# Optimization experiments

Hardware: AMD Instinct MI355X
Metric: run time of the kernel (lower is better)

## Reference

```python
import jax, jax.numpy as jnp
import numpy as np

B, V, S, H = 16384, 16, 64, 512


def setup_inputs() -> dict:
    key = jax.random.key(0)
    kx, kw, kb, kws, kbs = jax.random.split(key, 5)
    x = jax.random.normal(kx, (B, V, S), dtype=jnp.float32)
    # per-variable linear layers: weight [V, S, H], bias [V, H]
    W = jax.random.normal(kw, (V, S, H), dtype=jnp.float32) * (1.0 / np.sqrt(S))
    b = jax.random.normal(kb, (V, H), dtype=jnp.float32) * 0.01
    # variable selection linear: hidden -> V
    W_sel = jax.random.normal(kws, (H, V), dtype=jnp.float32) * (1.0 / np.sqrt(H))
    b_sel = jax.random.normal(kbs, (V,), dtype=jnp.float32) * 0.01
    return {"x": x, "W": W, "b": b, "W_sel": W_sel, "b_sel": b_sel}


def reference(x, W, b, W_sel, b_sel):
    # per-variable linears: [B, V, H]
    transformed = jnp.einsum('bvs,vsh->bvh', x, W) + b  # grouped small GEMMs
    # torch stacks to [B, H, V]; mean over variable axis -> [B, H]
    flat = transformed.mean(axis=1)
    # softmax-gated selection weights [B, V] (dropout is identity in eval)
    weights = jax.nn.softmax(flat @ W_sel + b_sel, axis=-1)
    # weighted sum over variables -> [B, H]
    out = jnp.einsum('bvh,bv->bh', transformed, weights)
    return out
```

## Files before the change

kernel.cpp:

```cpp
#include <hip/hip_runtime.h>
#include <hip/hip_bf16.h>
#include <stdint.h>

#define B_ROWS 16384
#define VDIM   16
#define SDIM   64
#define HDIM   512
#define KDIM   1024
#define KP     1056
#define ASTR   1064
#define K2_LDS (64 * ASTR * 2)

using bf16x8 = __attribute__((ext_vector_type(8))) __bf16;
using u16x8  = __attribute__((ext_vector_type(8))) unsigned short;
using f32x4  = __attribute__((ext_vector_type(4))) float;

__device__ __forceinline__ unsigned short f2bf(float f) {
  unsigned int u = __builtin_bit_cast(unsigned int, f);
  u = (u + 0x7FFFu + ((u >> 16) & 1u)) >> 16;
  return (unsigned short)u;
}

__global__ __launch_bounds__(256) void k0_prep(
    const float* __restrict__ W, const float* __restrict__ bias,
    const float* __restrict__ Wsel, const float* __restrict__ bsel,
    unsigned short* __restrict__ Bt, unsigned short* __restrict__ WcombT,
    float* __restrict__ bcomb) {
  __shared__ float wsl[512 * 17];
  __shared__ float bm[HDIM];
  __shared__ float part[16][17];
  const int t = threadIdx.x;
  if (blockIdx.x < 2112) {
    int idx = blockIdx.x * 256 + t;
    int k = idx >> 9;
    int n = idx & 511;
    float val;
    if (k < KDIM)            val = W[(size_t)k * HDIM + n];
    else if (k < KDIM + 16)  val = bias[(size_t)(k - KDIM) * HDIM + n];
    else                     val = 0.f;
    Bt[(size_t)n * KP + k] = f2bf(val);
    return;
  }
  const int bid = blockIdx.x - 2112;
  if (bid < 256) {
    for (int i = t; i < 512 * 16; i += 256) {
      int h = i >> 4, v = i & 15;
      wsl[h * 17 + v] = Wsel[i];
    }
    __syncthreads();
    const int wave = t >> 6, lane = t & 63;
    const int k = bid * 4 + wave;
    const float* wr = W + (size_t)k * HDIM;
    float s[16];
    #pragma unroll
    for (int v = 0; v < 16; ++v) s[v] = 0.f;
    #pragma unroll
    for (int j = 0; j < 8; ++j) {
      const int h = lane + 64 * j;
      const float a = wr[h];
      const float* wl = &wsl[h * 17];
      #pragma unroll
      for (int v = 0; v < 16; ++v) s[v] = fmaf(a, wl[v], s[v]);
    }
    #pragma unroll
    for (int off = 32; off > 0; off >>= 1) {
      #pragma unroll
      for (int v = 0; v < 16; ++v) s[v] += __shfl_xor(s[v], off, 64);
    }
    float mine = 0.f;
    #pragma unroll
    for (int v = 0; v < 16; ++v) mine = (lane == v) ? s[v] : mine;
    if (lane < 16) WcombT[lane * KDIM + k] = f2bf(mine * (1.f / 16.f));
  } else {
    for (int h = t; h < HDIM; h += 256) {
      float s = 0.f;
      #pragma unroll
      for (int v = 0; v < VDIM; ++v) s += bias[v * HDIM + h];
      bm[h] = s * (1.f / 16.f);
    }
    __syncthreads();
    int v = t & 15, sl = t >> 4;
    float s = 0.f;
    for (int h = sl * 32; h < sl * 32 + 32; ++h) s = fmaf(bm[h], Wsel[h * VDIM + v], s);
    part[sl][v] = s;
    __syncthreads();
    if (t < 16) {
      float s2 = bsel[t];
      #pragma unroll
      for (int i = 0; i < 16; ++i) s2 += part[i][t];
      bcomb[t] = s2;
    }
  }
}

__global__ __launch_bounds__(256) void k1a_logits(
    const float* __restrict__ x, const unsigned short* __restrict__ WcombT,
    float* __restrict__ part) {
  const int gw = blockIdx.x * 4 + (threadIdx.x >> 6);
  const int lane = threadIdx.x & 63;
  const int rt = gw >> 2, seg = gw & 3;
  const int m = lane & 15, quad = lane >> 4;
  const float* xr = x + (size_t)(rt * 16 + m) * KDIM + seg * 256 + quad * 8;
  const unsigned short* br = WcombT + m * KDIM + seg * 256 + quad * 8;
  f32x4 acc = {0.f, 0.f, 0.f, 0.f};
  #pragma unroll
  for (int kt = 0; kt < 8; ++kt) {
    float4 a0 = *(const float4*)(xr);
    float4 a1 = *(const float4*)(xr + 4);
    xr += 32;
    u16x8 u;
    u[0] = f2bf(a0.x); u[1] = f2bf(a0.y); u[2] = f2bf(a0.z); u[3] = f2bf(a0.w);
    u[4] = f2bf(a1.x); u[5] = f2bf(a1.y); u[6] = f2bf(a1.z); u[7] = f2bf(a1.w);
    bf16x8 af = __builtin_bit_cast(bf16x8, u);
    bf16x8 bfv = *(const bf16x8*)(br);
    br += 32;
    acc = __builtin_amdgcn_mfma_f32_16x16x32_bf16(af, bfv, acc, 0, 0, 0);
  }
  float* pr = part + (size_t)(rt * 16 + quad * 4) * 64 + seg * 16 + m;
  #pragma unroll
  for (int r = 0; r < 4; ++r) pr[(size_t)r * 64] = acc[r];
}

__global__ __launch_bounds__(256) void k1b0_softmax(
    const float* __restrict__ part, const float* __restrict__ bcomb,
    float* __restrict__ weights) {
  const int row = blockIdx.x * 256 + threadIdx.x;
  const float* p = part + (size_t)row * 64;
  float l[16];
  float mx = -1e30f;
  #pragma unroll
  for (int v = 0; v < 16; ++v) {
    l[v] = bcomb[v] + p[v] + p[16 + v] + p[32 + v] + p[48 + v];
    mx = fmaxf(mx, l[v]);
  }
  float s = 0.f;
  #pragma unroll
  for (int v = 0; v < 16; ++v) { l[v] = __expf(l[v] - mx); s += l[v]; }
  const float inv = 1.f / s;
  float4* wout = (float4*)(weights + (size_t)row * 16);
  #pragma unroll
  for (int q = 0; q < 4; ++q) {
    float4 f;
    f.x = l[4 * q + 0] * inv; f.y = l[4 * q + 1] * inv;
    f.z = l[4 * q + 2] * inv; f.w = l[4 * q + 3] * inv;
    wout[q] = f;
  }
}

__global__ __launch_bounds__(512, 2) void k2f_gemm(
    const float* __restrict__ x, const float* __restrict__ wts,
    const unsigned short* __restrict__ Bt, float* __restrict__ C) {
  extern __shared__ unsigned short As[];

  const int t = threadIdx.x;
  const int rowb = blockIdx.x * 64;

  {
    const int srow = t >> 3;
    const int sc = (t & 7) * 4;
    const float* xr = x + (size_t)(rowb + srow) * KDIM + sc;
    const float* wr = wts + (size_t)(rowb + srow) * 16;
    float wv[16];
    #pragma unroll
    for (int q = 0; q < 4; ++q) {
      float4 f = ((const float4*)wr)[q];
      wv[4 * q + 0] = f.x; wv[4 * q + 1] = f.y; wv[4 * q + 2] = f.z; wv[4 * q + 3] = f.w;
    }
    unsigned short* aw = As + srow * ASTR + sc;
    #pragma unroll 4
    for (int i = 0; i < 32; ++i) {
      const float4 a = *(const float4*)(xr + i * 32);
      const float w = wv[i >> 1];
      unsigned short o[4];
      o[0] = f2bf(w * a.x); o[1] = f2bf(w * a.y);
      o[2] = f2bf(w * a.z); o[3] = f2bf(w * a.w);
      *(uint2*)(aw + i * 32) = *(const uint2*)o;
    }
    if ((t & 7) < 4) {
      const int j8 = (t & 7) * 8;
      unsigned short o[8];
      #pragma unroll
      for (int jj = 0; jj < 8; ++jj)
        o[jj] = (j8 + jj < 16) ? f2bf(wv[j8 + jj]) : (unsigned short)0;
      *(u16x8*)(As + srow * ASTR + KDIM + j8) = *(const u16x8*)o;
    }
  }
  __syncthreads();

  const int wave = t >> 6, lane = t & 63;
  const int mlane = lane & 15, quad = lane >> 4;
  const int colb = wave * 64;

  const unsigned short* bp[4];
  #pragma unroll
  for (int j = 0; j < 4; ++j)
    bp[j] = Bt + (size_t)(colb + j * 16 + mlane) * KP + quad * 8;
  const unsigned short* ap[4];
  #pragma unroll
  for (int i = 0; i < 4; ++i)
    ap[i] = As + (i * 16 + mlane) * ASTR + quad * 8;

  f32x4 acc[4][4];
  const f32x4 z = {0.f, 0.f, 0.f, 0.f};
  #pragma unroll
  for (int i = 0; i < 4; ++i)
    #pragma unroll
    for (int j = 0; j < 4; ++j) acc[i][j] = z;

  #pragma unroll 1
  for (int kt = 0; kt < 33; ++kt) {
    bf16x8 bv[4], av[4];
    #pragma unroll
    for (int j = 0; j < 4; ++j) { bv[j] = *(const bf16x8*)bp[j]; bp[j] += 32; }
    #pragma unroll
    for (int i = 0; i < 4; ++i) { av[i] = *(const bf16x8*)ap[i]; ap[i] += 32; }
    #pragma unroll
    for (int i = 0; i < 4; ++i)
      #pragma unroll
      for (int j = 0; j < 4; ++j)
        acc[i][j] = __builtin_amdgcn_mfma_f32_16x16x32_bf16(av[i], bv[j], acc[i][j], 0, 0, 0);
  }

  #pragma unroll
  for (int i = 0; i < 4; ++i)
    #pragma unroll
    for (int j = 0; j < 4; ++j)
      #pragma unroll
      for (int r = 0; r < 4; ++r) {
        const size_t row = (size_t)rowb + i * 16 + quad * 4 + r;
        const int col = colb + j * 16 + mlane;
        C[row * HDIM + col] = acc[i][j][r];
      }
}

extern "C" void kernel_launch(void* const* d_in, const int* in_sizes, int n_in,
                              void* d_out, int out_size, void* d_ws, size_t ws_size,
                              hipStream_t stream) {
  const float* x    = (const float*)d_in[0];
  const float* W    = (const float*)d_in[1];
  const float* bias = (const float*)d_in[2];
  const float* Wsel = (const float*)d_in[3];
  const float* bsel = (const float*)d_in[4];
  float* out = (float*)d_out;

  char* ws = (char*)d_ws;
  unsigned short* Bt     = (unsigned short*)(ws);
  unsigned short* WcombT = (unsigned short*)(ws + 1081344);
  float*          bcomb  = (float*)(ws + 1114112);
  float*          part   = (float*)(ws + 1114368);
  float*          wts    = (float*)(ws + 5308672);

  static int lds_set = 0;
  if (!lds_set) {
    hipFuncSetAttribute((const void*)k2f_gemm,
                        hipFuncAttributeMaxDynamicSharedMemorySize, K2_LDS);
    lds_set = 1;
  }

  k0_prep<<<2369, 256, 0, stream>>>(W, bias, Wsel, bsel, Bt, WcombT, bcomb);
  k1a_logits<<<1024, 256, 0, stream>>>(x, WcombT, part);
  k1b0_softmax<<<64, 256, 0, stream>>>(part, bcomb, wts);
  k2f_gemm<<<256, 512, K2_LDS, stream>>>(x, wts, Bt, out);
}
```

Before: 163.5 us.

## Cache bf16 copy of x in logits pass and prefetch B operands in GEMM

The logits kernel now writes a bf16 copy of x to workspace, and the main GEMM reads that copy instead of re-reading fp32 x. This halves the second read of the 64MB input at the cost of a 32MB extra write, and double-rounds x (bf16 then scaled, then bf16 again). The GEMM also software-pipelines B-fragment global loads two steps ahead and moves the barrier after the initial B loads. The Wsel LDS staging in the prep kernel is replaced with direct float4 global loads.

```diff
diff --git a/kernel.cpp b/kernel.cpp
--- a/kernel.cpp
+++ b/kernel.cpp
@@ -20,13 +20,15 @@
   u = (u + 0x7FFFu + ((u >> 16) & 1u)) >> 16;
   return (unsigned short)u;
 }
+__device__ __forceinline__ float bf2f(unsigned short s) {
+  return __builtin_bit_cast(float, (unsigned int)s << 16);
+}
 
 __global__ __launch_bounds__(256) void k0_prep(
     const float* __restrict__ W, const float* __restrict__ bias,
     const float* __restrict__ Wsel, const float* __restrict__ bsel,
     unsigned short* __restrict__ Bt, unsigned short* __restrict__ WcombT,
     float* __restrict__ bcomb) {
-  __shared__ float wsl[512 * 17];
   __shared__ float bm[HDIM];
   __shared__ float part[16][17];
   const int t = threadIdx.x;
@@ -43,11 +45,6 @@
   }
   const int bid = blockIdx.x - 2112;
   if (bid < 256) {
-    for (int i = t; i < 512 * 16; i += 256) {
-      int h = i >> 4, v = i & 15;
-      wsl[h * 17 + v] = Wsel[i];
-    }
-    __syncthreads();
     const int wave = t >> 6, lane = t & 63;
     const int k = bid * 4 + wave;
     const float* wr = W + (size_t)k * HDIM;
@@ -58,9 +55,16 @@
     for (int j = 0; j < 8; ++j) {
       const int h = lane + 64 * j;
       const float a = wr[h];
-      const float* wl = &wsl[h * 17];
-      #pragma unroll
-      for (int v = 0; v < 16; ++v) s[v] = fmaf(a, wl[v], s[v]);
+      const float4* wl = (const float4*)(Wsel + h * 16);
+      const float4 q0 = wl[0], q1 = wl[1], q2 = wl[2], q3 = wl[3];
+      s[0]  = fmaf(a, q0.x, s[0]);  s[1]  = fmaf(a, q0.y, s[1]);
+      s[2]  = fmaf(a, q0.z, s[2]);  s[3]  = fmaf(a, q0.w, s[3]);
+      s[4]  = fmaf(a, q1.x, s[4]);  s[5]  = fmaf(a, q1.y, s[5]);
+      s[6]  = fmaf(a, q1.z, s[6]);  s[7]  = fmaf(a, q1.w, s[7]);
+      s[8]  = fmaf(a, q2.x, s[8]);  s[9]  = fmaf(a, q2.y, s[9]);
+      s[10] = fmaf(a, q2.z, s[10]); s[11] = fmaf(a, q2.w, s[11]);
+      s[12] = fmaf(a, q3.x, s[12]); s[13] = fmaf(a, q3.y, s[13]);
+      s[14] = fmaf(a, q3.z, s[14]); s[15] = fmaf(a, q3.w, s[15]);
     }
     #pragma unroll
     for (int off = 32; off > 0; off >>= 1) {
@@ -95,12 +99,14 @@
 
 __global__ __launch_bounds__(256) void k1a_logits(
     const float* __restrict__ x, const unsigned short* __restrict__ WcombT,
-    float* __restrict__ part) {
+    float* __restrict__ part, unsigned short* __restrict__ xb) {
   const int gw = blockIdx.x * 4 + (threadIdx.x >> 6);
   const int lane = threadIdx.x & 63;
   const int rt = gw >> 2, seg = gw & 3;
   const int m = lane & 15, quad = lane >> 4;
-  const float* xr = x + (size_t)(rt * 16 + m) * KDIM + seg * 256 + quad * 8;
+  const size_t off0 = (size_t)(rt * 16 + m) * KDIM + seg * 256 + quad * 8;
+  const float* xr = x + off0;
+  unsigned short* xw = xb + off0;
   const unsigned short* br = WcombT + m * KDIM + seg * 256 + quad * 8;
   f32x4 acc = {0.f, 0.f, 0.f, 0.f};
   #pragma unroll
@@ -111,6 +117,8 @@
     u16x8 u;
     u[0] = f2bf(a0.x); u[1] = f2bf(a0.y); u[2] = f2bf(a0.z); u[3] = f2bf(a0.w);
     u[4] = f2bf(a1.x); u[5] = f2bf(a1.y); u[6] = f2bf(a1.z); u[7] = f2bf(a1.w);
+    *(u16x8*)xw = u;
+    xw += 32;
     bf16x8 af = __builtin_bit_cast(bf16x8, u);
     bf16x8 bfv = *(const bf16x8*)(br);
     br += 32;
@@ -148,7 +156,7 @@
 }
 
 __global__ __launch_bounds__(512, 2) void k2f_gemm(
-    const float* __restrict__ x, const float* __restrict__ wts,
+    const unsigned short* __restrict__ xb, const float* __restrict__ wts,
     const unsigned short* __restrict__ Bt, float* __restrict__ C) {
   extern __shared__ unsigned short As[];
 
@@ -157,8 +165,8 @@
 
   {
     const int srow = t >> 3;
-    const int sc = (t & 7) * 4;
-    const float* xr = x + (size_t)(rowb + srow) * KDIM + sc;
+    const int sc = (t & 7) * 8;
+    const unsigned short* xr = xb + (size_t)(rowb + srow) * KDIM + sc;
     const float* wr = wts + (size_t)(rowb + srow) * 16;
     float wv[16];
     #pragma unroll
@@ -168,13 +176,13 @@
     }
     unsigned short* aw = As + srow * ASTR + sc;
     #pragma unroll 4
-    for (int i = 0; i < 32; ++i) {
-      const float4 a = *(const float4*)(xr + i * 32);
-      const float w = wv[i >> 1];
-      unsigned short o[4];
-      o[0] = f2bf(w * a.x); o[1] = f2bf(w * a.y);
-      o[2] = f2bf(w * a.z); o[3] = f2bf(w * a.w);
-      *(uint2*)(aw + i * 32) = *(const uint2*)o;
+    for (int i = 0; i < 16; ++i) {
+      const u16x8 a = *(const u16x8*)(xr + i * 64);
+      const float w = wv[i];
+      u16x8 o;
+      #pragma unroll
+      for (int j = 0; j < 8; ++j) o[j] = f2bf(w * bf2f(a[j]));
+      *(u16x8*)(aw + i * 64) = o;
     }
     if ((t & 7) < 4) {
       const int j8 = (t & 7) * 8;
@@ -185,7 +193,6 @@
       *(u16x8*)(As + srow * ASTR + KDIM + j8) = *(const u16x8*)o;
     }
   }
-  __syncthreads();
 
   const int wave = t >> 6, lane = t & 63;
   const int mlane = lane & 15, quad = lane >> 4;
@@ -195,6 +202,17 @@
   #pragma unroll
   for (int j = 0; j < 4; ++j)
     bp[j] = Bt + (size_t)(colb + j * 16 + mlane) * KP + quad * 8;
+
+  bf16x8 bv0[4], bv1[4];
+  #pragma unroll
+  for (int j = 0; j < 4; ++j) {
+    bv0[j] = *(const bf16x8*)(bp[j]);
+    bv1[j] = *(const bf16x8*)(bp[j] + 32);
+    bp[j] += 64;
+  }
+
+  __syncthreads();
+
   const unsigned short* ap[4];
   #pragma unroll
   for (int i = 0; i < 4; ++i)
@@ -209,16 +227,21 @@
 
   #pragma unroll 1
   for (int kt = 0; kt < 33; ++kt) {
-    bf16x8 bv[4], av[4];
-    #pragma unroll
-    for (int j = 0; j < 4; ++j) { bv[j] = *(const bf16x8*)bp[j]; bp[j] += 32; }
+    bf16x8 bnext[4];
+    if (kt < 31) {
+      #pragma unroll
+      for (int j = 0; j < 4; ++j) { bnext[j] = *(const bf16x8*)bp[j]; bp[j] += 32; }
+    }
+    bf16x8 av[4];
     #pragma unroll
     for (int i = 0; i < 4; ++i) { av[i] = *(const bf16x8*)ap[i]; ap[i] += 32; }
     #pragma unroll
     for (int i = 0; i < 4; ++i)
       #pragma unroll
       for (int j = 0; j < 4; ++j)
-        acc[i][j] = __builtin_amdgcn_mfma_f32_16x16x32_bf16(av[i], bv[j], acc[i][j], 0, 0, 0);
+        acc[i][j] = __builtin_amdgcn_mfma_f32_16x16x32_bf16(av[i], bv0[j], acc[i][j], 0, 0, 0);
+    #pragma unroll
+    for (int j = 0; j < 4; ++j) { bv0[j] = bv1[j]; bv1[j] = bnext[j]; }
   }
 
   #pragma unroll
@@ -249,6 +272,7 @@
   float*          bcomb  = (float*)(ws + 1114112);
   float*          part   = (float*)(ws + 1114368);
   float*          wts    = (float*)(ws + 5308672);
+  unsigned short* xbb    = (unsigned short*)(ws + 6357248);
 
   static int lds_set = 0;
   if (!lds_set) {
@@ -258,7 +282,7 @@
   }
 
   k0_prep<<<2369, 256, 0, stream>>>(W, bias, Wsel, bsel, Bt, WcombT, bcomb);
-  k1a_logits<<<1024, 256, 0, stream>>>(x, WcombT, part);
+  k1a_logits<<<1024, 256, 0, stream>>>(x, WcombT, part, xbb);
   k1b0_softmax<<<64, 256, 0, stream>>>(part, bcomb, wts);
-  k2f_gemm<<<256, 512, K2_LDS, stream>>>(x, wts, Bt, out);
-}
+  k2f_gemm<<<256, 512, K2_LDS, stream>>>(xbb, wts, Bt, out);
+}
```

Result: no change. 162.9 us (-0.4%).
